# Performance work log

Measured on AMD Instinct MI355X. Metric: run time of the kernel, lower is better.

The kernel has to match this reference:

```python
import jax, jax.numpy as jnp
import numpy as np
import math

B, S, D = 4, 2048, 1024
H, HD = 16, 64
RANK = 16
SCALING = 32.0 / RANK  # alpha / rank = 2.0


def setup_inputs() -> dict:
    key = jax.random.key(0)
    ks = jax.random.split(key, 12)
    s = 1.0 / math.sqrt(D)
    inp = {
        "hidden_states": jax.random.normal(ks[0], (B, S, D), dtype=jnp.float32),
        "attention_mask": jnp.zeros((B, 1, 1, S), dtype=jnp.float32),
        "Wq": jax.random.normal(ks[1], (D, D), dtype=jnp.float32) * s,
        "bq": jnp.zeros((D,), dtype=jnp.float32),
        "Aq": jax.random.normal(ks[2], (RANK, D), dtype=jnp.float32) * s,
        "Bq": jax.random.normal(ks[3], (D, RANK), dtype=jnp.float32) * 0.02,
        "Wk": jax.random.normal(ks[4], (D, D), dtype=jnp.float32) * s,
        "bk": jnp.zeros((D,), dtype=jnp.float32),
        "Wv": jax.random.normal(ks[5], (D, D), dtype=jnp.float32) * s,
        "bv": jnp.zeros((D,), dtype=jnp.float32),
        "Av": jax.random.normal(ks[6], (RANK, D), dtype=jnp.float32) * s,
        "Bv": jax.random.normal(ks[7], (D, RANK), dtype=jnp.float32) * 0.02,
        "Wo": jax.random.normal(ks[8], (D, D), dtype=jnp.float32) * s,
        "bo": jnp.zeros((D,), dtype=jnp.float32),
    }
    return inp


def _lora_linear(x, W, b, A, Bm):
    # F.linear(x, W, b) + (x @ A.T @ B.T) * scaling
    return x @ W.T + b + ((x @ A.T) @ Bm.T) * SCALING


def reference(hidden_states, attention_mask, Wq, bq, Aq, Bq, Wk, bk, Wv, bv, Av, Bv, Wo, bo):
    x = hidden_states
    q = _lora_linear(x, Wq, bq, Aq, Bq)          # [B,S,D]
    k = x @ Wk.T + bk                             # [B,S,D]
    v = _lora_linear(x, Wv, bv, Av, Bv)           # [B,S,D]

    def split_heads(t):
        return t.reshape(B, S, H, HD).transpose(0, 2, 1, 3)  # [B,H,S,HD]

    q, k, v = split_heads(q), split_heads(k), split_heads(v)
    scores = jnp.einsum("bhqd,bhkd->bhqk", q, k) / math.sqrt(HD)  # [B,H,S,S]
    scores = scores + attention_mask
    attn = jax.nn.softmax(scores, axis=-1)
    ctx = jnp.einsum("bhqk,bhkd->bhqd", attn, v)  # [B,H,S,HD]
    ctx = ctx.transpose(0, 2, 1, 3).reshape(B, S, D)
    return ctx @ Wo.T + bo
```

## Files before the change

kernel.cpp:

```cpp
#include <hip/hip_runtime.h>
#include <cstdint>


#define D_DIM 1024
#define S_DIM 2048
#define B_DIM 4
#define H_DIM 16
#define HD_DIM 64
#define M_DIM 8192
#define LOG2E 1.44269504f

typedef __bf16 bf16;
typedef unsigned int u32;
typedef __bf16 bf16x2v __attribute__((ext_vector_type(2)));
typedef __bf16 bf16x4v __attribute__((ext_vector_type(4)));
typedef __bf16 bf16x8 __attribute__((ext_vector_type(8)));
typedef float f32x4 __attribute__((ext_vector_type(4)));

typedef __attribute__((address_space(1))) void* as1p;
typedef __attribute__((address_space(3))) void* as3p;

__device__ __forceinline__ void gll16(const void* g, void* l) {
  __builtin_amdgcn_global_load_lds((as1p)(g), (as3p)(l), 16, 0, 0);
}

__device__ __forceinline__ u32 pack_bf16(float lo, float hi) {
  bf16x2v t;
  t[0] = (bf16)lo;
  t[1] = (bf16)hi;
  return __builtin_bit_cast(u32, t);
}

template <int TOTAL>
__device__ __forceinline__ int xcd_swz(int flat) {
  return (flat & 7) * (TOTAL >> 3) + (flat >> 3);
}

__global__ void convert_x_kernel(const float* __restrict__ x, bf16* __restrict__ xb) {
  const int i = (blockIdx.x * 256 + threadIdx.x) * 8;
  const float4 a = *(const float4*)(x + i);
  const float4 b = *(const float4*)(x + i + 4);
  bf16x8 o;
  o[0] = (bf16)a.x; o[1] = (bf16)a.y; o[2] = (bf16)a.z; o[3] = (bf16)a.w;
  o[4] = (bf16)b.x; o[5] = (bf16)b.y; o[6] = (bf16)b.z; o[7] = (bf16)b.w;
  *(bf16x8*)(xb + i) = o;
}

__global__ void prep_w_kernel(const float* __restrict__ W, const float* __restrict__ A,
                              const float* __restrict__ Bm, bf16* __restrict__ out,
                              int use_lora) {
  const int i = blockIdx.x * 256 + threadIdx.x;
  const int n = i >> 10, k = i & (D_DIM - 1);
  float w = W[i];
  if (use_lora) {
    float acc = 0.f;
#pragma unroll
    for (int r = 0; r < 16; ++r) acc = fmaf(Bm[n * 16 + r], A[r * D_DIM + k], acc);
    w += 2.0f * acc;
  }
  out[i] = (bf16)w;
}

__global__ __launch_bounds__(256) void gemm_qkv_kernel(
    const bf16* __restrict__ X, const bf16* __restrict__ Wqkv,
    const float* __restrict__ bq, const float* __restrict__ bk,
    const float* __restrict__ bv, bf16* __restrict__ Qo, bf16* __restrict__ Ko,
    bf16* __restrict__ Vo) {
  __shared__ __attribute__((aligned(16))) bf16 As[2][128 * 64];
  __shared__ __attribute__((aligned(16))) bf16 Bs[2][128 * 64];
  const int tid = threadIdx.x;
  const int wave = tid >> 6, lane = tid & 63;
  const int quad = lane >> 4, l16 = lane & 15;
  const int swz = xcd_swz<64 * 24>(blockIdx.y * 64 + blockIdx.x);
  const int m0 = (swz & 63) * 128, n0 = (swz >> 6) * 128;
  const int wm = (wave >> 1) * 64, wn = (wave & 1) * 64;
  const int srow = lane >> 3, sblk = lane & 7;

  const f32x4 zero = {0.f, 0.f, 0.f, 0.f};
  f32x4 acc[4][4];
#pragma unroll
  for (int mi = 0; mi < 4; ++mi)
#pragma unroll
    for (int ni = 0; ni < 4; ++ni) acc[mi][ni] = zero;

  auto stage = [&](int kt) {
    const int buf = kt & 1, kb = kt * 64;
#pragma unroll
    for (int it = 0; it < 4; ++it) {
      const int c = it * 4 + wave;
      const int row = c * 8 + srow;
      const int b = sblk ^ (row & 7);
      gll16(X + (size_t)(m0 + row) * D_DIM + kb + b * 8, &As[buf][c * 512 + lane * 8]);
      gll16(Wqkv + (size_t)(n0 + row) * D_DIM + kb + b * 8, &Bs[buf][c * 512 + lane * 8]);
    }
  };
  stage(0);

  for (int kt = 0; kt < D_DIM / 64; ++kt) {
    __syncthreads();
    if (kt + 1 < D_DIM / 64) stage(kt + 1);
    const bf16* as_ = &As[kt & 1][0];
    const bf16* bs_ = &Bs[kt & 1][0];
#pragma unroll
    for (int ks = 0; ks < 2; ++ks) {
      bf16x8 af[4], bfr[4];
#pragma unroll
      for (int mi = 0; mi < 4; ++mi) {
        const int row = wm + mi * 16 + l16;
        af[mi] = *(const bf16x8*)(as_ + row * 64 + (((ks * 4 + quad) ^ (row & 7)) * 8));
      }
#pragma unroll
      for (int ni = 0; ni < 4; ++ni) {
        const int row = wn + ni * 16 + l16;
        bfr[ni] = *(const bf16x8*)(bs_ + row * 64 + (((ks * 4 + quad) ^ (row & 7)) * 8));
      }
#pragma unroll
      for (int mi = 0; mi < 4; ++mi)
#pragma unroll
        for (int ni = 0; ni < 4; ++ni)
          acc[mi][ni] =
              __builtin_amdgcn_mfma_f32_16x16x32_bf16(af[mi], bfr[ni], acc[mi][ni], 0, 0, 0);
    }
  }

  const int sel = n0 >> 10;
  const float* bp = (sel == 0) ? bq : (sel == 1) ? bk : bv;
  const float qs = 0.125f * LOG2E;

  if (sel == 2) {
#pragma unroll
    for (int ni = 0; ni < 4; ++ni) {
      const int c = (n0 + wn + ni * 16 + l16) & 1023;
      const int h = c >> 6, hd = c & 63;
      const float bvv = bp[c];
#pragma unroll
      for (int mi = 0; mi < 4; ++mi) {
        const int row0 = m0 + wm + mi * 16 + quad * 4;
        const int b = row0 >> 11, s0 = row0 & (S_DIM - 1);
        bf16x4v pk;
#pragma unroll
        for (int r = 0; r < 4; ++r) pk[r] = (bf16)(acc[mi][ni][r] + bvv);
        *(bf16x4v*)(Vo + ((size_t)(b * H_DIM + h) * HD_DIM + hd) * S_DIM + s0) = pk;
      }
    }
  } else {
    bf16* O = (sel == 0) ? Qo : Ko;
#pragma unroll
    for (int ni = 0; ni < 4; ++ni) {
      const int c = (n0 + wn + ni * 16 + l16) & 1023;
      const int h = c >> 6, hd = c & 63;
      const float bvv = bp[c];
#pragma unroll
      for (int mi = 0; mi < 4; ++mi) {
#pragma unroll
        for (int r = 0; r < 4; ++r) {
          const int row = m0 + wm + mi * 16 + quad * 4 + r;
          const int b = row >> 11, s = row & (S_DIM - 1);
          float v = acc[mi][ni][r] + bvv;
          if (sel == 0) v *= qs;
          O[((size_t)(b * H_DIM + h) * S_DIM + s) * HD_DIM + hd] = (bf16)v;
        }
      }
    }
  }
}

__global__ __launch_bounds__(256) void gemm_o_kernel(const bf16* __restrict__ X,
                                                     const bf16* __restrict__ W,
                                                     const float* __restrict__ bias,
                                                     float* __restrict__ out) {
  __shared__ __attribute__((aligned(16))) bf16 As[2][128 * 64];
  __shared__ __attribute__((aligned(16))) bf16 Bs[2][128 * 64];
  const int tid = threadIdx.x;
  const int wave = tid >> 6, lane = tid & 63;
  const int quad = lane >> 4, l16 = lane & 15;
  const int swz = xcd_swz<64 * 8>(blockIdx.y * 64 + blockIdx.x);
  const int m0 = (swz & 63) * 128, n0 = (swz >> 6) * 128;
  const int wm = (wave >> 1) * 64, wn = (wave & 1) * 64;
  const int srow = lane >> 3, sblk = lane & 7;

  const f32x4 zero = {0.f, 0.f, 0.f, 0.f};
  f32x4 acc[4][4];
#pragma unroll
  for (int mi = 0; mi < 4; ++mi)
#pragma unroll
    for (int ni = 0; ni < 4; ++ni) acc[mi][ni] = zero;

  auto stage = [&](int kt) {
    const int buf = kt & 1, kb = kt * 64;
#pragma unroll
    for (int it = 0; it < 4; ++it) {
      const int c = it * 4 + wave;
      const int row = c * 8 + srow;
      const int b = sblk ^ (row & 7);
      gll16(X + (size_t)(m0 + row) * D_DIM + kb + b * 8, &As[buf][c * 512 + lane * 8]);
      gll16(W + (size_t)(n0 + row) * D_DIM + kb + b * 8, &Bs[buf][c * 512 + lane * 8]);
    }
  };
  stage(0);

  for (int kt = 0; kt < D_DIM / 64; ++kt) {
    __syncthreads();
    if (kt + 1 < D_DIM / 64) stage(kt + 1);
    const bf16* as_ = &As[kt & 1][0];
    const bf16* bs_ = &Bs[kt & 1][0];
#pragma unroll
    for (int ks = 0; ks < 2; ++ks) {
      bf16x8 af[4], bfr[4];
#pragma unroll
      for (int mi = 0; mi < 4; ++mi) {
        const int row = wm + mi * 16 + l16;
        af[mi] = *(const bf16x8*)(as_ + row * 64 + (((ks * 4 + quad) ^ (row & 7)) * 8));
      }
#pragma unroll
      for (int ni = 0; ni < 4; ++ni) {
        const int row = wn + ni * 16 + l16;
        bfr[ni] = *(const bf16x8*)(bs_ + row * 64 + (((ks * 4 + quad) ^ (row & 7)) * 8));
      }
#pragma unroll
      for (int mi = 0; mi < 4; ++mi)
#pragma unroll
        for (int ni = 0; ni < 4; ++ni)
          acc[mi][ni] =
              __builtin_amdgcn_mfma_f32_16x16x32_bf16(af[mi], bfr[ni], acc[mi][ni], 0, 0, 0);
    }
  }
#pragma unroll
  for (int ni = 0; ni < 4; ++ni) {
    const int col = n0 + wn + ni * 16 + l16;
    const float bv = bias[col];
#pragma unroll
    for (int mi = 0; mi < 4; ++mi)
#pragma unroll
      for (int r = 0; r < 4; ++r) {
        const int row = m0 + wm + mi * 16 + quad * 4 + r;
        out[(size_t)row * D_DIM + col] = acc[mi][ni][r] + bv;
      }
  }
}

__global__ __launch_bounds__(512, 4) void attn_kernel(const bf16* __restrict__ Q,
                                                      const bf16* __restrict__ K,
                                                      const bf16* __restrict__ Vt,
                                                      const float* __restrict__ mask,
                                                      bf16* __restrict__ ctx) {
  __shared__ __attribute__((aligned(16))) bf16 Ks[2][64 * 64];
  __shared__ __attribute__((aligned(16))) bf16 Vs[2][64 * 64];
  __shared__ __attribute__((aligned(16))) float cms[S_DIM];

  const int tid = threadIdx.x;
  const int wave = tid >> 6, lane = tid & 63;
  const int quad = lane >> 4, l16 = lane & 15;
  const int swz = xcd_swz<512>(blockIdx.y * 8 + blockIdx.x);
  const int bh = swz >> 3, b = bh >> 4, h = bh & 15;
  const int qt = swz & 7;

  const bf16* Qg = Q + ((size_t)bh * S_DIM + qt * 256 + wave * 32) * HD_DIM;
  bf16x8 qf[2][2];
#pragma unroll
  for (int nq = 0; nq < 2; ++nq)
#pragma unroll
    for (int ks = 0; ks < 2; ++ks)
      qf[nq][ks] = *(const bf16x8*)(Qg + (nq * 16 + l16) * HD_DIM + ks * 32 + quad * 8);

  {
    const float* mp = mask + b * S_DIM + tid * 4;
    const float4 a = *(const float4*)(mp);
    f32x4 r0 = {fmaf(a.x, LOG2E, -16.f), fmaf(a.y, LOG2E, -16.f),
                fmaf(a.z, LOG2E, -16.f), fmaf(a.w, LOG2E, -16.f)};
    *(f32x4*)(cms + tid * 4) = r0;
  }

  bf16x8 onef;
#pragma unroll
  for (int j = 0; j < 8; ++j) onef[j] = (bf16)1.0f;

  const f32x4 zero = {0.f, 0.f, 0.f, 0.f};
  f32x4 o[2][4], osum[2];
#pragma unroll
  for (int nq = 0; nq < 2; ++nq) {
    osum[nq] = zero;
#pragma unroll
    for (int nh = 0; nh < 4; ++nh) o[nq][nh] = zero;
  }

  const bf16* Kg0 = K + (size_t)bh * S_DIM * HD_DIM;
  const bf16* Vg0 = Vt + (size_t)bh * HD_DIM * S_DIM;

  auto stage = [&](int t) {
    const int buf = t & 1;
    const bf16* Kg = Kg0 + (size_t)t * 64 * HD_DIM;
    const bf16* Vg = Vg0 + t * 64;
    const int c = wave;
    const int row = c * 8 + (lane >> 3);
    const int blk = (lane & 7) ^ (row & 7);
    gll16(Kg + (size_t)row * HD_DIM + blk * 8, &Ks[buf][c * 512 + lane * 8]);
    gll16(Vg + (size_t)row * S_DIM + blk * 8, &Vs[buf][c * 512 + lane * 8]);
  };
  stage(0);

  for (int t = 0; t < S_DIM / 64; ++t) {
    __syncthreads();
    if (t + 1 < S_DIM / 64) stage(t + 1);
    const bf16* ks_ = &Ks[t & 1][0];
    const bf16* vs_ = &Vs[t & 1][0];

#pragma unroll
    for (int half = 0; half < 2; ++half) {
      u32 pk[2][2][2];
#pragma unroll
      for (int mtl = 0; mtl < 2; ++mtl) {
        const int mt = half * 2 + mtl;
        const f32x4 cm = *(const f32x4*)(cms + t * 64 + mt * 16 + quad * 4);
        f32x4 sc[2];
        sc[0] = cm;
        sc[1] = cm;
#pragma unroll
        for (int ks = 0; ks < 2; ++ks) {
          const int row = mt * 16 + l16;
          const bf16x8 kf =
              *(const bf16x8*)(ks_ + row * 64 + (((ks * 4 + quad) ^ (row & 7)) * 8));
#pragma unroll
          for (int nq = 0; nq < 2; ++nq)
            sc[nq] = __builtin_amdgcn_mfma_f32_16x16x32_bf16(kf, qf[nq][ks], sc[nq], 0, 0, 0);
        }
#pragma unroll
        for (int nq = 0; nq < 2; ++nq) {
          const float e0 = __builtin_amdgcn_exp2f(sc[nq][0]);
          const float e1 = __builtin_amdgcn_exp2f(sc[nq][1]);
          const float e2 = __builtin_amdgcn_exp2f(sc[nq][2]);
          const float e3 = __builtin_amdgcn_exp2f(sc[nq][3]);
          pk[nq][mtl][0] = pack_bf16(e0, e1);
          pk[nq][mtl][1] = pack_bf16(e2, e3);
        }
      }

      bf16x8 vf[4];
#pragma unroll
      for (int nh = 0; nh < 4; ++nh) {
        const int vrow = nh * 16 + l16;
        vf[nh] = *(const bf16x8*)(vs_ + vrow * 64 + (((half * 4 + quad) ^ (vrow & 7)) * 8));
      }

#pragma unroll
      for (int nq = 0; nq < 2; ++nq) {
        auto a0 = __builtin_amdgcn_permlane32_swap(pk[nq][0][0], pk[nq][1][0], false, false);
        auto a1 = __builtin_amdgcn_permlane32_swap(pk[nq][0][1], pk[nq][1][1], false, false);
        auto b0 = __builtin_amdgcn_permlane16_swap(a0[0], a0[1], false, false);
        auto b1 = __builtin_amdgcn_permlane16_swap(a1[0], a1[1], false, false);
        union {
          u32 w[4];
          bf16x8 v;
        } pu;
        pu.w[0] = b0[0];
        pu.w[1] = b1[0];
        pu.w[2] = b0[1];
        pu.w[3] = b1[1];
        const bf16x8 pf = pu.v;
#pragma unroll
        for (int nh = 0; nh < 4; ++nh)
          o[nq][nh] = __builtin_amdgcn_mfma_f32_16x16x32_bf16(pf, vf[nh], o[nq][nh], 0, 0, 0);
        osum[nq] = __builtin_amdgcn_mfma_f32_16x16x32_bf16(pf, onef, osum[nq], 0, 0, 0);
      }
    }
  }

#pragma unroll
  for (int nq = 0; nq < 2; ++nq)
#pragma unroll
    for (int r = 0; r < 4; ++r) {
      const float inv = 1.0f / osum[nq][r];
      const int s = qt * 256 + wave * 32 + nq * 16 + quad * 4 + r;
#pragma unroll
      for (int nh = 0; nh < 4; ++nh)
        ctx[((size_t)b * S_DIM + s) * D_DIM + h * 64 + nh * 16 + l16] =
            (bf16)(o[nq][nh][r] * inv);
    }
}

extern "C" void kernel_launch(void* const* d_in, const int* in_sizes, int n_in,
                              void* d_out, int out_size, void* d_ws, size_t ws_size,
                              hipStream_t stream) {
  const float* x    = (const float*)d_in[0];
  const float* mask = (const float*)d_in[1];
  const float* Wq   = (const float*)d_in[2];
  const float* bq   = (const float*)d_in[3];
  const float* Aq   = (const float*)d_in[4];
  const float* Bq   = (const float*)d_in[5];
  const float* Wk   = (const float*)d_in[6];
  const float* bk   = (const float*)d_in[7];
  const float* Wv   = (const float*)d_in[8];
  const float* bv   = (const float*)d_in[9];
  const float* Av   = (const float*)d_in[10];
  const float* Bv   = (const float*)d_in[11];
  const float* Wo   = (const float*)d_in[12];
  const float* bo   = (const float*)d_in[13];
  float* out = (float*)d_out;

  bf16* xb   = (bf16*)d_ws;
  bf16* wqkv = xb + (size_t)M_DIM * D_DIM;
  bf16* wo   = wqkv + (size_t)3 * D_DIM * D_DIM;
  bf16* Qw   = wo + (size_t)D_DIM * D_DIM;
  bf16* Kw   = Qw + (size_t)M_DIM * D_DIM;
  bf16* Vw   = Kw + (size_t)M_DIM * D_DIM;
  bf16* Cw   = xb;

  convert_x_kernel<<<M_DIM * D_DIM / (256 * 8), 256, 0, stream>>>(x, xb);
  prep_w_kernel<<<D_DIM * D_DIM / 256, 256, 0, stream>>>(Wq, Aq, Bq, wqkv, 1);
  prep_w_kernel<<<D_DIM * D_DIM / 256, 256, 0, stream>>>(Wk, nullptr, nullptr,
                                                         wqkv + (size_t)D_DIM * D_DIM, 0);
  prep_w_kernel<<<D_DIM * D_DIM / 256, 256, 0, stream>>>(Wv, Av, Bv,
                                                         wqkv + (size_t)2 * D_DIM * D_DIM, 1);
  prep_w_kernel<<<D_DIM * D_DIM / 256, 256, 0, stream>>>(Wo, nullptr, nullptr, wo, 0);

  gemm_qkv_kernel<<<dim3(M_DIM / 128, 3 * D_DIM / 128), 256, 0, stream>>>(
      xb, wqkv, bq, bk, bv, Qw, Kw, Vw);

  attn_kernel<<<dim3(S_DIM / 256, B_DIM * H_DIM), 512, 0, stream>>>(Qw, Kw, Vw, mask, Cw);

  gemm_o_kernel<<<dim3(M_DIM / 128, D_DIM / 128), 256, 0, stream>>>(Cw, wo, bo, out);
}
```

Baseline: 306.9 us.

## Merge weight-prep launches into one kernel and drop XCD block swizzle

Replaces the four per-matrix weight preparation launches with a single kernel that selects the source matrix from the block index, cutting launch overhead and the tail effects of several small grids. Separately, both projection GEMMs drop the XCD-aware block swizzle and map blockIdx directly to tile coordinates. The second change may hurt L2 locality across chiplets, because neighbouring tiles that share operand rows will now land on different XCDs.

```diff
diff --git a/kernel.cpp b/kernel.cpp
--- a/kernel.cpp
+++ b/kernel.cpp
@@ -46,18 +46,26 @@
   *(bf16x8*)(xb + i) = o;
 }
 
-__global__ void prep_w_kernel(const float* __restrict__ W, const float* __restrict__ A,
-                              const float* __restrict__ Bm, bf16* __restrict__ out,
-                              int use_lora) {
-  const int i = blockIdx.x * 256 + threadIdx.x;
+__global__ void prep_w_all_kernel(const float* __restrict__ Wq, const float* __restrict__ Aq,
+                                  const float* __restrict__ Bq, const float* __restrict__ Wk,
+                                  const float* __restrict__ Wv, const float* __restrict__ Av,
+                                  const float* __restrict__ Bv, const float* __restrict__ Wo,
+                                  bf16* __restrict__ wqkv, bf16* __restrict__ wo) {
+  const int blk = blockIdx.x;
+  const int sel = blk >> 12;
+  const int i = (blk & 4095) * 256 + threadIdx.x;
   const int n = i >> 10, k = i & (D_DIM - 1);
+  const float* W = (sel == 0) ? Wq : (sel == 1) ? Wk : (sel == 2) ? Wv : Wo;
   float w = W[i];
-  if (use_lora) {
+  if (sel == 0 || sel == 2) {
+    const float* A = (sel == 0) ? Aq : Av;
+    const float* Bm = (sel == 0) ? Bq : Bv;
     float acc = 0.f;
 #pragma unroll
     for (int r = 0; r < 16; ++r) acc = fmaf(Bm[n * 16 + r], A[r * D_DIM + k], acc);
     w += 2.0f * acc;
   }
+  bf16* out = (sel == 3) ? wo : wqkv + (size_t)sel * D_DIM * D_DIM;
   out[i] = (bf16)w;
 }
 
@@ -71,8 +79,7 @@
   const int tid = threadIdx.x;
   const int wave = tid >> 6, lane = tid & 63;
   const int quad = lane >> 4, l16 = lane & 15;
-  const int swz = xcd_swz<64 * 24>(blockIdx.y * 64 + blockIdx.x);
-  const int m0 = (swz & 63) * 128, n0 = (swz >> 6) * 128;
+  const int m0 = blockIdx.x * 128, n0 = blockIdx.y * 128;
   const int wm = (wave >> 1) * 64, wn = (wave & 1) * 64;
   const int srow = lane >> 3, sblk = lane & 7;
 
@@ -174,8 +181,7 @@
   const int tid = threadIdx.x;
   const int wave = tid >> 6, lane = tid & 63;
   const int quad = lane >> 4, l16 = lane & 15;
-  const int swz = xcd_swz<64 * 8>(blockIdx.y * 64 + blockIdx.x);
-  const int m0 = (swz & 63) * 128, n0 = (swz >> 6) * 128;
+  const int m0 = blockIdx.x * 128, n0 = blockIdx.y * 128;
   const int wm = (wave >> 1) * 64, wn = (wave & 1) * 64;
   const int srow = lane >> 3, sblk = lane & 7;
 
@@ -406,12 +412,8 @@
   bf16* Cw   = xb;
 
   convert_x_kernel<<<M_DIM * D_DIM / (256 * 8), 256, 0, stream>>>(x, xb);
-  prep_w_kernel<<<D_DIM * D_DIM / 256, 256, 0, stream>>>(Wq, Aq, Bq, wqkv, 1);
-  prep_w_kernel<<<D_DIM * D_DIM / 256, 256, 0, stream>>>(Wk, nullptr, nullptr,
-                                                         wqkv + (size_t)D_DIM * D_DIM, 0);
-  prep_w_kernel<<<D_DIM * D_DIM / 256, 256, 0, stream>>>(Wv, Av, Bv,
-                                                         wqkv + (size_t)2 * D_DIM * D_DIM, 1);
-  prep_w_kernel<<<D_DIM * D_DIM / 256, 256, 0, stream>>>(Wo, nullptr, nullptr, wo, 0);
+  prep_w_all_kernel<<<4 * D_DIM * D_DIM / 256, 256, 0, stream>>>(
+      Wq, Aq, Bq, Wk, Wv, Av, Bv, Wo, wqkv, wo);
 
   gemm_qkv_kernel<<<dim3(M_DIM / 128, 3 * D_DIM / 128), 256, 0, stream>>>(
       xb, wqkv, bq, bk, bv, Qw, Kw, Vw);
```

Result: faster. 282.1 us (-8.1%).
